# Optimization experiments

Hardware: AMD Instinct MI355X
Metric: run time of the kernel (lower is better)

The kernel has to match this reference:

```python
import jax, jax.numpy as jnp
import numpy as np

B, N, C = 4, 2048, 512
H = 8
HD = C // H  # 64
SCALE = HD ** -0.5


def setup_inputs() -> dict:
    key = jax.random.key(0)
    k1, k2, k3 = jax.random.split(key, 3)
    x = jax.random.normal(k1, (B, N, C), dtype=jnp.float32)
    w_qkv = jax.random.normal(k2, (3 * C, C), dtype=jnp.float32) * (C ** -0.5)
    b_qkv = jnp.zeros((3 * C,), dtype=jnp.float32)
    w_proj = jax.random.normal(k3, (C, C), dtype=jnp.float32) * (C ** -0.5)
    b_proj = jnp.zeros((C,), dtype=jnp.float32)
    return {"x": x, "w_qkv": w_qkv, "b_qkv": b_qkv, "w_proj": w_proj, "b_proj": b_proj}


def reference(x, w_qkv, b_qkv, w_proj, b_proj):
    # qkv projection: (B,N,C) @ (C,3C) -> (B,N,3,H,HD) -> (3,B,H,N,HD)
    qkv = (x @ w_qkv.T + b_qkv).reshape(B, N, 3, H, HD).transpose(2, 0, 3, 1, 4)
    q, k, v = qkv[0], qkv[1], qkv[2]
    # scores (B,H,N,N), scale applied after matmul as in the torch source
    attn = jnp.einsum('bhnd,bhmd->bhnm', q, k) * SCALE
    attn = jax.nn.softmax(attn, axis=-1)
    out = jnp.einsum('bhnm,bhmd->bhnd', attn, v)  # (B,H,N,HD)
    out = out.transpose(0, 2, 1, 3).reshape(B, N, C)
    return out @ w_proj.T + b_proj
```

## Files before the change

### kernel.cpp

```cpp
#include <hip/hip_runtime.h>

#define B_ 4
#define N_ 2048
#define C_ 512
#define H_ 8
#define HD_ 64
#define SCALE_ 0.125f
#define QSCALE_ 0.18033688011112042f

typedef __attribute__((ext_vector_type(8))) __bf16 bf16x8;
typedef __attribute__((ext_vector_type(4))) float f32x4;
typedef __attribute__((ext_vector_type(4))) unsigned int u32x4;
typedef __attribute__((ext_vector_type(2))) unsigned int u32x2;

__device__ __forceinline__ unsigned short f2bf(float f) {
    unsigned int u = __builtin_bit_cast(unsigned int, f);
    u += 0x7fffu + ((u >> 16) & 1u);
    return (unsigned short)(u >> 16);
}

__device__ __forceinline__ void llds16(const void* g, void* l) {
    __builtin_amdgcn_global_load_lds(
        (const __attribute__((address_space(1))) unsigned int*)g,
        (__attribute__((address_space(3))) unsigned int*)l, 16, 0, 0);
}

__global__ __launch_bounds__(256) void cvt_all(const float* __restrict__ x,
                                               const float* __restrict__ wq,
                                               const float* __restrict__ wp,
                                               unsigned short* __restrict__ xb,
                                               unsigned short* __restrict__ wqb,
                                               unsigned short* __restrict__ wpb) {
    const int NX = B_ * N_ * C_ / 4, NQ = 3 * C_ * C_ / 4, NP = C_ * C_ / 4;
    int i = blockIdx.x * 256 + threadIdx.x;
    const float4* src;
    ushort4* dst;
    int idx;
    if (i < NX) { src = (const float4*)x; dst = (ushort4*)xb; idx = i; }
    else if (i < NX + NQ) { src = (const float4*)wq; dst = (ushort4*)wqb; idx = i - NX; }
    else if (i < NX + NQ + NP) { src = (const float4*)wp; dst = (ushort4*)wpb; idx = i - NX - NQ; }
    else return;
    float4 v = src[idx];
    ushort4 o;
    o.x = f2bf(v.x); o.y = f2bf(v.y); o.z = f2bf(v.z); o.w = f2bf(v.w);
    dst[idx] = o;
}

template <int MODE>
__global__ __launch_bounds__(256) void gemm_bt(const unsigned short* __restrict__ A,
                                               const unsigned short* __restrict__ Bw,
                                               const float* __restrict__ bias,
                                               float* __restrict__ Out,
                                               unsigned short* __restrict__ Qb,
                                               unsigned short* __restrict__ Kb,
                                               unsigned short* __restrict__ Vt) {
    constexpr int K = 512;
    __shared__ __align__(16) unsigned char smem[32768];
    unsigned char* sA = smem;
    unsigned char* sB = smem + 16384;

    const int tid = threadIdx.x;
    const int lane = tid & 63;
    const int wave = tid >> 6;
    const int wm = wave >> 1, wn = wave & 1;
    const int m0 = blockIdx.y * 128;
    const int n0 = blockIdx.x * 128;

    f32x4 acc[4][4] = {};

    for (int k0 = 0; k0 < K; k0 += 64) {
#pragma unroll
        for (int i = 0; i < 4; i++) {
            int ci = wave * 4 + i;
            int row = ci * 8 + (lane >> 3);
            int cb = (lane & 7) * 16;
            const unsigned char* ga =
                (const unsigned char*)A + ((size_t)(m0 + row) * K + k0) * 2 + cb;
            const unsigned char* gb =
                (const unsigned char*)Bw + ((size_t)(n0 + row) * K + k0) * 2 + cb;
            llds16(ga, sA + ci * 1024);
            llds16(gb, sB + ci * 1024);
        }
        __syncthreads();
#pragma unroll
        for (int kk = 0; kk < 2; kk++) {
            bf16x8 af[4], bfr[4];
#pragma unroll
            for (int mi = 0; mi < 4; mi++)
                af[mi] = *(const bf16x8*)(sA + (wm * 64 + mi * 16 + (lane & 15)) * 128 +
                                          kk * 64 + (lane >> 4) * 16);
#pragma unroll
            for (int ni = 0; ni < 4; ni++)
                bfr[ni] = *(const bf16x8*)(sB + (wn * 64 + ni * 16 + (lane & 15)) * 128 +
                                           kk * 64 + (lane >> 4) * 16);
#pragma unroll
            for (int mi = 0; mi < 4; mi++)
#pragma unroll
                for (int ni = 0; ni < 4; ni++)
                    acc[mi][ni] = __builtin_amdgcn_mfma_f32_16x16x32_bf16(
                        af[mi], bfr[ni], acc[mi][ni], 0, 0, 0);
        }
        __syncthreads();
    }

    if constexpr (MODE == 0) {
#pragma unroll
        for (int ni = 0; ni < 4; ni++) {
            int c = n0 + wn * 64 + ni * 16 + (lane & 15);
            int sel = c >> 9, h = (c >> 6) & 7, d = c & 63;
            float bv = bias[c];
#pragma unroll
            for (int mi = 0; mi < 4; mi++) {
#pragma unroll
                for (int r = 0; r < 4; r++) {
                    int m = m0 + wm * 64 + mi * 16 + ((lane >> 4) << 2) + r;
                    int b = m >> 11, n = m & (N_ - 1);
                    float fv = acc[mi][ni][r] + bv;
                    if (sel == 0) {
                        Qb[((size_t)(b * H_ + h) * N_ + n) * HD_ + d] = f2bf(fv * QSCALE_);
                    } else if (sel == 1) {
                        Kb[((size_t)(b * H_ + h) * N_ + n) * HD_ + d] = f2bf(fv);
                    } else {
                        Vt[((size_t)(b * H_ + h) * HD_ + d) * (size_t)N_ + n] = f2bf(fv);
                    }
                }
            }
        }
    } else {
#pragma unroll
        for (int ni = 0; ni < 4; ni++) {
            int c = n0 + wn * 64 + ni * 16 + (lane & 15);
            float bv = bias[c];
#pragma unroll
            for (int mi = 0; mi < 4; mi++) {
#pragma unroll
                for (int r = 0; r < 4; r++) {
                    int m = m0 + wm * 64 + mi * 16 + ((lane >> 4) << 2) + r;
                    Out[(size_t)m * C_ + c] = acc[mi][ni][r] + bv;
                }
            }
        }
    }
}

__global__ __launch_bounds__(512, 4) void attn_fwd(const unsigned short* __restrict__ Qb,
                                                   const unsigned short* __restrict__ Kb,
                                                   const unsigned short* __restrict__ Vt,
                                                   unsigned short* __restrict__ AO) {
    __shared__ __align__(16) unsigned char smem[49152];

    const int tid = threadIdx.x, lane = tid & 63, wave = tid >> 6;
    const int g = lane >> 4, c = lane & 15;
    const int bh = blockIdx.y;
    const int q0 = blockIdx.x * 128 + wave * 16;
    const unsigned short* Qh = Qb + (size_t)bh * N_ * HD_;
    const unsigned short* Kh = Kb + (size_t)bh * N_ * HD_;
    const unsigned short* Vh = Vt + (size_t)bh * HD_ * N_;
    unsigned char* sPT = smem + 32768 + wave * 2048;
    unsigned char* ptw = sPT + c * 32 + g * 8;
    const unsigned int ptr32 = (unsigned int)(size_t)sPT + g * 256 + c * 8;

    bf16x8 qf[2];
#pragma unroll
    for (int kk = 0; kk < 2; kk++)
        qf[kk] = *(const bf16x8*)(Qh + (size_t)(q0 + c) * HD_ + kk * 32 + g * 8);

    bf16x8 ones;
#pragma unroll
    for (int i = 0; i < 8; i++) ones[i] = (__bf16)1.0f;

    f32x4 o[4] = {};
    f32x4 osum = {};

    const int srow = tid >> 3;
    const int sslot = (tid & 7) * 16;
    const int ssw = (sslot ^ ((srow & 7) << 4));

    {
        u32x4 kreg = *(const u32x4*)((const unsigned char*)Kh + (size_t)srow * 128 + sslot);
        u32x4 vreg = *(const u32x4*)((const unsigned char*)Vh + (size_t)srow * (N_ * 2) + sslot);
        *(u32x4*)(smem + srow * 128 + ssw) = kreg;
        *(u32x4*)(smem + 16384 + srow * 128 + ssw) = vreg;
    }
    __syncthreads();

#pragma unroll 1
    for (int t = 0; t < N_ / 64; t++) {
        unsigned char* bK = smem + (t & 1) * 8192;
        unsigned char* bV = smem + 16384 + (t & 1) * 8192;

        u32x4 kreg, vreg;
        if (t < N_ / 64 - 1) {
            int kv0 = (t + 1) * 64;
            kreg = *(const u32x4*)((const unsigned char*)Kh + (size_t)(kv0 + srow) * 128 + sslot);
            vreg = *(const u32x4*)((const unsigned char*)Vh + (size_t)srow * (N_ * 2) +
                                   kv0 * 2 + sslot);
        }

        f32x4 s[4] = {};
#pragma unroll
        for (int j = 0; j < 4; j++) {
#pragma unroll
            for (int kk = 0; kk < 2; kk++) {
                int krow = j * 16 + c;
                bf16x8 bf = *(const bf16x8*)(bK + krow * 128 +
                                             ((kk * 64 + g * 16) ^ ((krow & 7) << 4)));
                s[j] = __builtin_amdgcn_mfma_f32_16x16x32_bf16(qf[kk], bf, s[j], 0, 0, 0);
            }
        }

#pragma unroll
        for (int j = 0; j < 4; j++) {
            float p0 = __builtin_exp2f(s[j][0]);
            float p1 = __builtin_exp2f(s[j][1]);
            float p2 = __builtin_exp2f(s[j][2]);
            float p3 = __builtin_exp2f(s[j][3]);
            unsigned int lo, hi;
            asm("v_cvt_pk_bf16_f32 %0, %1, %2" : "=v"(lo) : "v"(p0), "v"(p1));
            asm("v_cvt_pk_bf16_f32 %0, %1, %2" : "=v"(hi) : "v"(p2), "v"(p3));
            u32x2 w;
            w[0] = lo;
            w[1] = hi;
            *(u32x2*)(ptw + j * 512) = w;
        }

        asm volatile("s_waitcnt lgkmcnt(0)" ::: "memory");
        __builtin_amdgcn_sched_barrier(0);

#pragma unroll
        for (int kk = 0; kk < 2; kk++) {
            u32x2 t0, t1;
            asm volatile("ds_read_b64_tr_b16 %0, %2\n\t"
                         "ds_read_b64_tr_b16 %1, %2 offset:128"
                         : "=v"(t0), "=v"(t1)
                         : "v"(ptr32 + kk * 1024)
                         : "memory");
            asm volatile("s_waitcnt lgkmcnt(0)");
            __builtin_amdgcn_sched_barrier(0);
            u32x4 wq;
            wq[0] = t0[0]; wq[1] = t0[1]; wq[2] = t1[0]; wq[3] = t1[1];
            bf16x8 pf = __builtin_bit_cast(bf16x8, wq);
            osum = __builtin_amdgcn_mfma_f32_16x16x32_bf16(pf, ones, osum, 0, 0, 0);
#pragma unroll
            for (int dj = 0; dj < 4; dj++) {
                int vrow = dj * 16 + c;
                bf16x8 vf = *(const bf16x8*)(bV + vrow * 128 +
                                             ((kk * 64 + g * 16) ^ ((vrow & 7) << 4)));
                o[dj] = __builtin_amdgcn_mfma_f32_16x16x32_bf16(pf, vf, o[dj], 0, 0, 0);
            }
        }

        if (t < N_ / 64 - 1) {
            unsigned char* nK = smem + ((t + 1) & 1) * 8192;
            unsigned char* nV = smem + 16384 + ((t + 1) & 1) * 8192;
            *(u32x4*)(nK + srow * 128 + ssw) = kreg;
            *(u32x4*)(nV + srow * 128 + ssw) = vreg;
        }
        __syncthreads();
    }

    const int b = bh >> 3, h = bh & 7;
#pragma unroll
    for (int r = 0; r < 4; r++) {
        float inv = 1.0f / osum[r];
        int n = q0 + (g << 2) + r;
#pragma unroll
        for (int dj = 0; dj < 4; dj++) {
            int col = h * HD_ + dj * 16 + c;
            AO[((size_t)(b * N_ + n)) * C_ + col] = f2bf(o[dj][r] * inv);
        }
    }
}

extern "C" void kernel_launch(void* const* d_in, const int* in_sizes, int n_in,
                              void* d_out, int out_size, void* d_ws, size_t ws_size,
                              hipStream_t stream) {
    const float* x = (const float*)d_in[0];
    const float* w_qkv = (const float*)d_in[1];
    const float* b_qkv = (const float*)d_in[2];
    const float* w_proj = (const float*)d_in[3];
    const float* b_proj = (const float*)d_in[4];
    float* out = (float*)d_out;

    unsigned char* ws = (unsigned char*)d_ws;
    unsigned short* xb = (unsigned short*)ws;
    unsigned short* AO = xb;
    unsigned short* wqb = (unsigned short*)(ws + 8388608);
    unsigned short* wpb = (unsigned short*)(ws + 8388608 + 1572864);
    unsigned short* Vt = (unsigned short*)(ws + 8388608 + 1572864 + 524288);

    unsigned short* Qb = (unsigned short*)d_out;
    unsigned short* Kb = Qb + (size_t)B_ * H_ * N_ * HD_;

    const int NALL = (B_ * N_ * C_ + 3 * C_ * C_ + C_ * C_) / 4;
    cvt_all<<<(NALL + 255) / 256, 256, 0, stream>>>(x, w_qkv, w_proj, xb, wqb, wpb);

    gemm_bt<0><<<dim3(12, 64), 256, 0, stream>>>(xb, wqb, b_qkv, nullptr, Qb, Kb, Vt);
    attn_fwd<<<dim3(16, 32), 512, 0, stream>>>(Qb, Kb, Vt, AO);
    gemm_bt<1><<<dim3(4, 64), 256, 0, stream>>>(AO, wpb, b_proj, out, nullptr, nullptr, nullptr);
}
```

Before: 126.6 us.

## Process two 16-row query tiles per wave in attention to reuse K/V fragments

Each wave now computes 32 query rows (two 16-row MFMA tiles) against the same K and V fragments read from LDS, and the block shrinks from 8 to 4 waves covering the same 128 queries. This halves LDS fragment reads per MFMA and each thread now stages two K/V rows per tile. In exchange, accumulator and score registers double and there are fewer waves per block to hide latency, with launch bounds relaxed to (256,3).

Result: slower. 131.8 us (+4.1%).

```diff
diff --git a/kernel.cpp b/kernel.cpp
--- a/kernel.cpp
+++ b/kernel.cpp
@@ -143,7 +143,7 @@
     }
 }
 
-__global__ __launch_bounds__(512, 4) void attn_fwd(const unsigned short* __restrict__ Qb,
+__global__ __launch_bounds__(256, 3) void attn_fwd(const unsigned short* __restrict__ Qb,
                                                    const unsigned short* __restrict__ Kb,
                                                    const unsigned short* __restrict__ Vt,
                                                    unsigned short* __restrict__ AO) {
@@ -152,35 +152,43 @@
     const int tid = threadIdx.x, lane = tid & 63, wave = tid >> 6;
     const int g = lane >> 4, c = lane & 15;
     const int bh = blockIdx.y;
-    const int q0 = blockIdx.x * 128 + wave * 16;
+    const int q0 = blockIdx.x * 128 + wave * 32;
     const unsigned short* Qh = Qb + (size_t)bh * N_ * HD_;
     const unsigned short* Kh = Kb + (size_t)bh * N_ * HD_;
     const unsigned short* Vh = Vt + (size_t)bh * HD_ * N_;
-    unsigned char* sPT = smem + 32768 + wave * 2048;
+    unsigned char* sPT = smem + 32768 + wave * 4096;
     unsigned char* ptw = sPT + c * 32 + g * 8;
     const unsigned int ptr32 = (unsigned int)(size_t)sPT + g * 256 + c * 8;
 
-    bf16x8 qf[2];
-#pragma unroll
-    for (int kk = 0; kk < 2; kk++)
-        qf[kk] = *(const bf16x8*)(Qh + (size_t)(q0 + c) * HD_ + kk * 32 + g * 8);
+    bf16x8 qf[2][2];
+#pragma unroll
+    for (int u = 0; u < 2; u++)
+#pragma unroll
+        for (int kk = 0; kk < 2; kk++)
+            qf[u][kk] = *(const bf16x8*)(Qh + (size_t)(q0 + u * 16 + c) * HD_ +
+                                         kk * 32 + g * 8);
 
     bf16x8 ones;
 #pragma unroll
     for (int i = 0; i < 8; i++) ones[i] = (__bf16)1.0f;
 
-    f32x4 o[4] = {};
-    f32x4 osum = {};
-
-    const int srow = tid >> 3;
+    f32x4 o[2][4] = {};
+    f32x4 osum[2] = {};
+
+    const int srow0 = tid >> 3, srow1 = (256 + tid) >> 3;
     const int sslot = (tid & 7) * 16;
-    const int ssw = (sslot ^ ((srow & 7) << 4));
+    const int ssw0 = (sslot ^ ((srow0 & 7) << 4));
+    const int ssw1 = (sslot ^ ((srow1 & 7) << 4));
 
     {
-        u32x4 kreg = *(const u32x4*)((const unsigned char*)Kh + (size_t)srow * 128 + sslot);
-        u32x4 vreg = *(const u32x4*)((const unsigned char*)Vh + (size_t)srow * (N_ * 2) + sslot);
-        *(u32x4*)(smem + srow * 128 + ssw) = kreg;
-        *(u32x4*)(smem + 16384 + srow * 128 + ssw) = vreg;
+        u32x4 k0 = *(const u32x4*)((const unsigned char*)Kh + (size_t)srow0 * 128 + sslot);
+        u32x4 k1 = *(const u32x4*)((const unsigned char*)Kh + (size_t)srow1 * 128 + sslot);
+        u32x4 v0 = *(const u32x4*)((const unsigned char*)Vh + (size_t)srow0 * (N_ * 2) + sslot);
+        u32x4 v1 = *(const u32x4*)((const unsigned char*)Vh + (size_t)srow1 * (N_ * 2) + sslot);
+        *(u32x4*)(smem + srow0 * 128 + ssw0) = k0;
+        *(u32x4*)(smem + srow1 * 128 + ssw1) = k1;
+        *(u32x4*)(smem + 16384 + srow0 * 128 + ssw0) = v0;
+        *(u32x4*)(smem + 16384 + srow1 * 128 + ssw1) = v1;
     }
     __syncthreads();
 
@@ -189,15 +197,18 @@
         unsigned char* bK = smem + (t & 1) * 8192;
         unsigned char* bV = smem + 16384 + (t & 1) * 8192;
 
-        u32x4 kreg, vreg;
+        u32x4 kreg0, kreg1, vreg0, vreg1;
         if (t < N_ / 64 - 1) {
             int kv0 = (t + 1) * 64;
-            kreg = *(const u32x4*)((const unsigned char*)Kh + (size_t)(kv0 + srow) * 128 + sslot);
-            vreg = *(const u32x4*)((const unsigned char*)Vh + (size_t)srow * (N_ * 2) +
-                                   kv0 * 2 + sslot);
-        }
-
-        f32x4 s[4] = {};
+            kreg0 = *(const u32x4*)((const unsigned char*)Kh + (size_t)(kv0 + srow0) * 128 + sslot);
+            kreg1 = *(const u32x4*)((const unsigned char*)Kh + (size_t)(kv0 + srow1) * 128 + sslot);
+            vreg0 = *(const u32x4*)((const unsigned char*)Vh + (size_t)srow0 * (N_ * 2) +
+                                    kv0 * 2 + sslot);
+            vreg1 = *(const u32x4*)((const unsigned char*)Vh + (size_t)srow1 * (N_ * 2) +
+                                    kv0 * 2 + sslot);
+        }
+
+        f32x4 s[2][4] = {};
 #pragma unroll
         for (int j = 0; j < 4; j++) {
 #pragma unroll
@@ -205,71 +216,87 @@
                 int krow = j * 16 + c;
                 bf16x8 bf = *(const bf16x8*)(bK + krow * 128 +
                                              ((kk * 64 + g * 16) ^ ((krow & 7) << 4)));
-                s[j] = __builtin_amdgcn_mfma_f32_16x16x32_bf16(qf[kk], bf, s[j], 0, 0, 0);
-            }
-        }
-
-#pragma unroll
-        for (int j = 0; j < 4; j++) {
-            float p0 = __builtin_exp2f(s[j][0]);
-            float p1 = __builtin_exp2f(s[j][1]);
-            float p2 = __builtin_exp2f(s[j][2]);
-            float p3 = __builtin_exp2f(s[j][3]);
-            unsigned int lo, hi;
-            asm("v_cvt_pk_bf16_f32 %0, %1, %2" : "=v"(lo) : "v"(p0), "v"(p1));
-            asm("v_cvt_pk_bf16_f32 %0, %1, %2" : "=v"(hi) : "v"(p2), "v"(p3));
-            u32x2 w;
-            w[0] = lo;
-            w[1] = hi;
-            *(u32x2*)(ptw + j * 512) = w;
-        }
+                s[0][j] = __builtin_amdgcn_mfma_f32_16x16x32_bf16(qf[0][kk], bf, s[0][j], 0, 0, 0);
+                s[1][j] = __builtin_amdgcn_mfma_f32_16x16x32_bf16(qf[1][kk], bf, s[1][j], 0, 0, 0);
+            }
+        }
+
+#pragma unroll
+        for (int u = 0; u < 2; u++)
+#pragma unroll
+            for (int j = 0; j < 4; j++) {
+                float p0 = __builtin_exp2f(s[u][j][0]);
+                float p1 = __builtin_exp2f(s[u][j][1]);
+                float p2 = __builtin_exp2f(s[u][j][2]);
+                float p3 = __builtin_exp2f(s[u][j][3]);
+                unsigned int lo, hi;
+                asm("v_cvt_pk_bf16_f32 %0, %1, %2" : "=v"(lo) : "v"(p0), "v"(p1));
+                asm("v_cvt_pk_bf16_f32 %0, %1, %2" : "=v"(hi) : "v"(p2), "v"(p3));
+                u32x2 w;
+                w[0] = lo;
+                w[1] = hi;
+                *(u32x2*)(ptw + u * 2048 + j * 512) = w;
+            }
 
         asm volatile("s_waitcnt lgkmcnt(0)" ::: "memory");
         __builtin_amdgcn_sched_barrier(0);
 
 #pragma unroll
         for (int kk = 0; kk < 2; kk++) {
-            u32x2 t0, t1;
+            u32x2 t00, t01, t10, t11;
             asm volatile("ds_read_b64_tr_b16 %0, %2\n\t"
                          "ds_read_b64_tr_b16 %1, %2 offset:128"
-                         : "=v"(t0), "=v"(t1)
+                         : "=v"(t00), "=v"(t01)
                          : "v"(ptr32 + kk * 1024)
+                         : "memory");
+            asm volatile("ds_read_b64_tr_b16 %0, %2\n\t"
+                         "ds_read_b64_tr_b16 %1, %2 offset:128"
+                         : "=v"(t10), "=v"(t11)
+                         : "v"(ptr32 + 2048 + kk * 1024)
                          : "memory");
             asm volatile("s_waitcnt lgkmcnt(0)");
             __builtin_amdgcn_sched_barrier(0);
-            u32x4 wq;
-            wq[0] = t0[0]; wq[1] = t0[1]; wq[2] = t1[0]; wq[3] = t1[1];
-            bf16x8 pf = __builtin_bit_cast(bf16x8, wq);
-            osum = __builtin_amdgcn_mfma_f32_16x16x32_bf16(pf, ones, osum, 0, 0, 0);
+            u32x4 w0, w1;
+            w0[0] = t00[0]; w0[1] = t00[1]; w0[2] = t01[0]; w0[3] = t01[1];
+            w1[0] = t10[0]; w1[1] = t10[1]; w1[2] = t11[0]; w1[3] = t11[1];
+            bf16x8 pf0 = __builtin_bit_cast(bf16x8, w0);
+            bf16x8 pf1 = __builtin_bit_cast(bf16x8, w1);
+            osum[0] = __builtin_amdgcn_mfma_f32_16x16x32_bf16(pf0, ones, osum[0], 0, 0, 0);
+            osum[1] = __builtin_amdgcn_mfma_f32_16x16x32_bf16(pf1, ones, osum[1], 0, 0, 0);
 #pragma unroll
             for (int dj = 0; dj < 4; dj++) {
                 int vrow = dj * 16 + c;
                 bf16x8 vf = *(const bf16x8*)(bV + vrow * 128 +
                                              ((kk * 64 + g * 16) ^ ((vrow & 7) << 4)));
-                o[dj] = __builtin_amdgcn_mfma_f32_16x16x32_bf16(pf, vf, o[dj], 0, 0, 0);
+                o[0][dj] = __builtin_amdgcn_mfma_f32_16x16x32_bf16(pf0, vf, o[0][dj], 0, 0, 0);
+                o[1][dj] = __builtin_amdgcn_mfma_f32_16x16x32_bf16(pf1, vf, o[1][dj], 0, 0, 0);
             }
         }
 
         if (t < N_ / 64 - 1) {
             unsigned char* nK = smem + ((t + 1) & 1) * 8192;
             unsigned char* nV = smem + 16384 + ((t + 1) & 1) * 8192;
-            *(u32x4*)(nK + srow * 128 + ssw) = kreg;
-            *(u32x4*)(nV + srow * 128 + ssw) = vreg;
+            *(u32x4*)(nK + srow0 * 128 + ssw0) = kreg0;
+            *(u32x4*)(nK + srow1 * 128 + ssw1) = kreg1;
+            *(u32x4*)(nV + srow0 * 128 + ssw0) = vreg0;
+            *(u32x4*)(nV + srow1 * 128 + ssw1) = vreg1;
         }
         __syncthreads();
     }
 
     const int b = bh >> 3, h = bh & 7;
 #pragma unroll
-    for (int r = 0; r < 4; r++) {
-        float inv = 1.0f / osum[r];
-        int n = q0 + (g << 2) + r;
-#pragma unroll
-        for (int dj = 0; dj < 4; dj++) {
-            int col = h * HD_ + dj * 16 + c;
-            AO[((size_t)(b * N_ + n)) * C_ + col] = f2bf(o[dj][r] * inv);
-        }
-    }
+    for (int u = 0; u < 2; u++)
+#pragma unroll
+        for (int r = 0; r < 4; r++) {
+            float inv = 1.0f / osum[u][r];
+            int n = q0 + u * 16 + (g << 2) + r;
+#pragma unroll
+            for (int dj = 0; dj < 4; dj++) {
+                int col = h * HD_ + dj * 16 + c;
+                AO[((size_t)(b * N_ + n)) * C_ + col] = f2bf(o[u][dj][r] * inv);
+            }
+        }
 }
 
 extern "C" void kernel_launch(void* const* d_in, const int* in_sizes, int n_in,
@@ -296,6 +323,6 @@
     cvt_all<<<(NALL + 255) / 256, 256, 0, stream>>>(x, w_qkv, w_proj, xb, wqb, wpb);
 
     gemm_bt<0><<<dim3(12, 64), 256, 0, stream>>>(xb, wqb, b_qkv, nullptr, Qb, Kb, Vt);
-    attn_fwd<<<dim3(16, 32), 512, 0, stream>>>(Qb, Kb, Vt, AO);
+    attn_fwd<<<dim3(16, 32), 256, 0, stream>>>(Qb, Kb, Vt, AO);
     gemm_bt<1><<<dim3(4, 64), 256, 0, stream>>>(AO, wpb, b_proj, out, nullptr, nullptr, nullptr);
 }
```

## Compute transposed scores to feed P directly from registers into 16x16x16 MFMAs

Applied to the files above, without the earlier changes.

Swaps the operand order of the QK^T MFMA so each lane holds score values laid out as the A operand of a 16x16x16 bf16 MFMA. The P tile is then fed straight from registers into the PV and row-sum MFMAs. This removes the per-wave LDS round trip (write, wait, transposed read) and cuts shared memory from 48KB to 32KB. In exchange it issues twice as many half-width MFMAs with 8-byte V reads, which may lower MFMA throughput per instruction.

New measurement: 131.6 us. +3.9%, slower.

```diff
diff --git a/kernel.cpp b/kernel.cpp
--- a/kernel.cpp
+++ b/kernel.cpp
@@ -12,6 +12,14 @@
 typedef __attribute__((ext_vector_type(4))) float f32x4;
 typedef __attribute__((ext_vector_type(4))) unsigned int u32x4;
 typedef __attribute__((ext_vector_type(2))) unsigned int u32x2;
+typedef __attribute__((ext_vector_type(4))) short s16x4;
+
+#if __has_builtin(__builtin_amdgcn_mfma_f32_16x16x16bf16_1k)
+#define MFMA16(acc, a, b) acc = __builtin_amdgcn_mfma_f32_16x16x16bf16_1k(a, b, acc, 0, 0, 0)
+#else
+#define MFMA16(acc, a, b) \
+    asm("v_mfma_f32_16x16x16_bf16 %0, %1, %2, %0" : "+v"(acc) : "v"(a), "v"(b))
+#endif
 
 __device__ __forceinline__ unsigned short f2bf(float f) {
     unsigned int u = __builtin_bit_cast(unsigned int, f);
@@ -147,7 +155,7 @@
                                                    const unsigned short* __restrict__ Kb,
                                                    const unsigned short* __restrict__ Vt,
                                                    unsigned short* __restrict__ AO) {
-    __shared__ __align__(16) unsigned char smem[49152];
+    __shared__ __align__(16) unsigned char smem[32768];
 
     const int tid = threadIdx.x, lane = tid & 63, wave = tid >> 6;
     const int g = lane >> 4, c = lane & 15;
@@ -156,18 +164,15 @@
     const unsigned short* Qh = Qb + (size_t)bh * N_ * HD_;
     const unsigned short* Kh = Kb + (size_t)bh * N_ * HD_;
     const unsigned short* Vh = Vt + (size_t)bh * HD_ * N_;
-    unsigned char* sPT = smem + 32768 + wave * 2048;
-    unsigned char* ptw = sPT + c * 32 + g * 8;
-    const unsigned int ptr32 = (unsigned int)(size_t)sPT + g * 256 + c * 8;
 
     bf16x8 qf[2];
 #pragma unroll
     for (int kk = 0; kk < 2; kk++)
         qf[kk] = *(const bf16x8*)(Qh + (size_t)(q0 + c) * HD_ + kk * 32 + g * 8);
 
-    bf16x8 ones;
-#pragma unroll
-    for (int i = 0; i < 8; i++) ones[i] = (__bf16)1.0f;
+    s16x4 ones16;
+#pragma unroll
+    for (int i = 0; i < 4; i++) ones16[i] = (short)0x3F80;
 
     f32x4 o[4] = {};
     f32x4 osum = {};
@@ -203,12 +208,13 @@
 #pragma unroll
             for (int kk = 0; kk < 2; kk++) {
                 int krow = j * 16 + c;
-                bf16x8 bf = *(const bf16x8*)(bK + krow * 128 +
+                bf16x8 kf = *(const bf16x8*)(bK + krow * 128 +
                                              ((kk * 64 + g * 16) ^ ((krow & 7) << 4)));
-                s[j] = __builtin_amdgcn_mfma_f32_16x16x32_bf16(qf[kk], bf, s[j], 0, 0, 0);
-            }
-        }
-
+                s[j] = __builtin_amdgcn_mfma_f32_16x16x32_bf16(kf, qf[kk], s[j], 0, 0, 0);
+            }
+        }
+
+        s16x4 pa[4];
 #pragma unroll
         for (int j = 0; j < 4; j++) {
             float p0 = __builtin_exp2f(s[j][0]);
@@ -221,32 +227,19 @@
             u32x2 w;
             w[0] = lo;
             w[1] = hi;
-            *(u32x2*)(ptw + j * 512) = w;
-        }
-
-        asm volatile("s_waitcnt lgkmcnt(0)" ::: "memory");
-        __builtin_amdgcn_sched_barrier(0);
-
-#pragma unroll
-        for (int kk = 0; kk < 2; kk++) {
-            u32x2 t0, t1;
-            asm volatile("ds_read_b64_tr_b16 %0, %2\n\t"
-                         "ds_read_b64_tr_b16 %1, %2 offset:128"
-                         : "=v"(t0), "=v"(t1)
-                         : "v"(ptr32 + kk * 1024)
-                         : "memory");
-            asm volatile("s_waitcnt lgkmcnt(0)");
-            __builtin_amdgcn_sched_barrier(0);
-            u32x4 wq;
-            wq[0] = t0[0]; wq[1] = t0[1]; wq[2] = t1[0]; wq[3] = t1[1];
-            bf16x8 pf = __builtin_bit_cast(bf16x8, wq);
-            osum = __builtin_amdgcn_mfma_f32_16x16x32_bf16(pf, ones, osum, 0, 0, 0);
+            pa[j] = __builtin_bit_cast(s16x4, w);
+        }
+
+#pragma unroll
+        for (int j = 0; j < 4; j++) {
+            MFMA16(osum, pa[j], ones16);
 #pragma unroll
             for (int dj = 0; dj < 4; dj++) {
                 int vrow = dj * 16 + c;
-                bf16x8 vf = *(const bf16x8*)(bV + vrow * 128 +
-                                             ((kk * 64 + g * 16) ^ ((vrow & 7) << 4)));
-                o[dj] = __builtin_amdgcn_mfma_f32_16x16x32_bf16(pf, vf, o[dj], 0, 0, 0);
+                u32x2 vv = *(const u32x2*)(bV + vrow * 128 +
+                                           ((j * 32 + 8 * g) ^ ((vrow & 7) << 4)));
+                s16x4 vfj = __builtin_bit_cast(s16x4, vv);
+                MFMA16(o[dj], pa[j], vfj);
             }
         }
 
```
